# Kernel tuning notes

Hardware: AMD Instinct MI355X
Metric: run time of the kernel (lower is better)

## Reference

```python
import jax, jax.numpy as jnp
import numpy as np

D_MODEL = 2048
NUM_HEADS = 16
D_K = D_MODEL // NUM_HEADS  # 128
BATCH, SEQ = 2, 2048


def setup_inputs() -> dict:
    key = jax.random.key(0)
    ks = jax.random.split(key, 9)
    s = 0.02
    return {
        "x": jax.random.normal(ks[0], (BATCH, SEQ, D_MODEL), dtype=jnp.float32),
        "W_q": jax.random.normal(ks[1], (D_MODEL, D_MODEL), dtype=jnp.float32) * s,
        "b_q": jax.random.normal(ks[2], (D_MODEL,), dtype=jnp.float32) * s,
        "W_k": jax.random.normal(ks[3], (D_MODEL, D_K), dtype=jnp.float32) * s,
        "b_k": jax.random.normal(ks[4], (D_K,), dtype=jnp.float32) * s,
        "W_v": jax.random.normal(ks[5], (D_MODEL, D_K), dtype=jnp.float32) * s,
        "b_v": jax.random.normal(ks[6], (D_K,), dtype=jnp.float32) * s,
        "W_o": jax.random.normal(ks[7], (D_MODEL, D_MODEL), dtype=jnp.float32) * s,
        "b_o": jax.random.normal(ks[8], (D_MODEL,), dtype=jnp.float32) * s,
    }


def reference(x, W_q, b_q, W_k, b_k, W_v, b_v, W_o, b_o):
    B, S, _ = x.shape
    # Q: per-head projections -> (B, H, S, d_k)
    Q = (x @ W_q + b_q).reshape(B, S, NUM_HEADS, D_K).transpose(0, 2, 1, 3)
    # K, V: single shared head -> (B, S, d_k)
    K = x @ W_k + b_k
    V = x @ W_v + b_v
    scale = 1.0 / np.sqrt(D_K)
    # scores: (B, H, S_q, S_k); K broadcast across heads (no expand materialized)
    scores = jnp.einsum("bhqd,bkd->bhqk", Q, K) * scale
    attn = jax.nn.softmax(scores, axis=-1)
    out = jnp.einsum("bhqk,bkd->bhqd", attn, V)  # (B, H, S, d_k)
    out = out.transpose(0, 2, 1, 3).reshape(B, S, D_MODEL)
    out = out @ W_o + b_o
    K_cache = K[:, None, :, :]  # (B, 1, S, d_k)
    V_cache = V[:, None, :, :]
    return (out, K_cache, V_cache)
```

## Files before the change

kernel.cpp:

```cpp
#include <hip/hip_runtime.h>
#include <cstdint>

typedef __bf16 bf16x8 __attribute__((ext_vector_type(8)));
typedef float f32x4 __attribute__((ext_vector_type(4)));
typedef unsigned short ushort_t;

constexpr int kS  = 2048;
constexpr int kDM = 2048;
constexpr int kDK = 128;
constexpr int kNH = 16;
constexpr int kB  = 2;
constexpr int kNQKV = kDM + 2 * kDK;

__device__ __forceinline__ unsigned short f2bf(float f) {
  union { float f; unsigned u; } v; v.f = f;
  unsigned u = v.u;
  u += 0x7fffu + ((u >> 16) & 1u);
  return (unsigned short)(u >> 16);
}

__device__ __forceinline__ void gload16(const void* g, void* l) {
  __builtin_amdgcn_global_load_lds(
      (const __attribute__((address_space(1))) void*)g,
      (__attribute__((address_space(3))) void*)l, 16, 0, 0);
}

__device__ __forceinline__ void xcd_swizzle(int& bx, int& by) {
  int gx = gridDim.x;
  int nwg = gx * gridDim.y;
  int id = by * gx + bx;
  int cpx = nwg >> 3;
  int sw = (id & 7) * cpx + (id >> 3);
  bx = sw % gx;
  by = sw / gx;
}

__global__ __launch_bounds__(256) void cast_f32_bf16(const float* __restrict__ in,
                                                     ushort_t* __restrict__ out, long n) {
  long i = ((long)blockIdx.x * 256 + threadIdx.x) * 4;
  if (i >= n) return;
  float4 f = *reinterpret_cast<const float4*>(in + i);
  ushort4 o;
  o.x = f2bf(f.x); o.y = f2bf(f.y); o.z = f2bf(f.z); o.w = f2bf(f.w);
  *reinterpret_cast<ushort4*>(out + i) = o;
}

__global__ __launch_bounds__(256) void transpose_cast(const float* __restrict__ in,
                                                      ushort_t* __restrict__ out,
                                                      int R, int C) {
  __shared__ float tile[32][33];
  int c = blockIdx.x * 32 + threadIdx.x;
  int r0 = blockIdx.y * 32;
  #pragma unroll
  for (int i = threadIdx.y; i < 32; i += 8)
    tile[i][threadIdx.x] = in[(long)(r0 + i) * C + c];
  __syncthreads();
  int oc  = r0 + threadIdx.x;
  int or0 = blockIdx.x * 32;
  #pragma unroll
  for (int i = threadIdx.y; i < 32; i += 8)
    out[(long)(or0 + i) * R + oc] = f2bf(tile[threadIdx.x][i]);
}

__device__ __forceinline__ void gemm128(const ushort_t* __restrict__ A, int lda,
                                        const ushort_t* __restrict__ Bt, int ldb,
                                        int K, int row0, int col0,
                                        f32x4 (&acc)[4][4]) {
  __shared__ __align__(16) ushort_t sA[2][128 * 32];
  __shared__ __align__(16) ushort_t sB[2][128 * 32];
  int t = threadIdx.x;
  int r = t >> 2, c4 = t & 3;
  const ushort_t* gA0 = A  + (long)(row0 + r)      * lda + c4 * 8;
  const ushort_t* gA1 = A  + (long)(row0 + r + 64) * lda + c4 * 8;
  const ushort_t* gB0 = Bt + (long)(col0 + r)      * ldb + c4 * 8;
  const ushort_t* gB1 = Bt + (long)(col0 + r + 64) * ldb + c4 * 8;
  int lane = t & 63, wave = t >> 6;
  int wr = wave >> 1, wc = wave & 1;
  int lr = lane & 15, lg = lane >> 4;
  int aoff = (wr * 64 + lr) * 32 + lg * 8;
  int boff = (wc * 64 + lr) * 32 + lg * 8;

  auto stage = [&](int kk, int bb) {
    gload16(gA0 + kk, (void*)(sA[bb] + t * 8));
    gload16(gA1 + kk, (void*)(sA[bb] + 2048 + t * 8));
    gload16(gB0 + kk, (void*)(sB[bb] + t * 8));
    gload16(gB1 + kk, (void*)(sB[bb] + 2048 + t * 8));
  };
  auto comp = [&](int bb) {
    bf16x8 af[4], bg[4];
    #pragma unroll
    for (int i = 0; i < 4; i++) af[i] = *(const bf16x8*)(sA[bb] + aoff + i * 16 * 32);
    #pragma unroll
    for (int j = 0; j < 4; j++) bg[j] = *(const bf16x8*)(sB[bb] + boff + j * 16 * 32);
    #pragma unroll
    for (int i = 0; i < 4; i++)
      #pragma unroll
      for (int j = 0; j < 4; j++)
        acc[i][j] = __builtin_amdgcn_mfma_f32_16x16x32_bf16(af[i], bg[j], acc[i][j], 0, 0, 0);
  };

  stage(0, 0);
  __syncthreads();
  for (int kk = 0; kk < K; kk += 64) {
    stage(kk + 32, 1);
    comp(0);
    __syncthreads();
    if (kk + 64 < K) stage(kk + 64, 0);
    comp(1);
    __syncthreads();
  }
}

__global__ __launch_bounds__(256) void gemm_qkv(const ushort_t* __restrict__ x,
    const ushort_t* __restrict__ Wt, const float* __restrict__ bq,
    const float* __restrict__ bk, const float* __restrict__ bv,
    ushort_t* __restrict__ Qb, float* __restrict__ Kc,
    ushort_t* __restrict__ Kb, float* __restrict__ Vc, ushort_t* __restrict__ Vtb) {
  f32x4 acc[4][4] = {};
  int bx = blockIdx.x, by = blockIdx.y;
  xcd_swizzle(bx, by);
  int row0 = by * 128, col0 = bx * 128;
  gemm128(x, kDM, Wt, kDM, kDM, row0, col0, acc);
  int lane = threadIdx.x & 63, wave = threadIdx.x >> 6;
  int wr = wave >> 1, wc = wave & 1, lr = lane & 15, lg = lane >> 4;
  #pragma unroll
  for (int i = 0; i < 4; i++) {
    #pragma unroll
    for (int j = 0; j < 4; j++) {
      int col = col0 + wc * 64 + j * 16 + lr;
      float bias = (col < kDM) ? bq[col]
                 : (col < kDM + kDK) ? bk[col - kDM] : bv[col - kDM - kDK];
      #pragma unroll
      for (int rr = 0; rr < 4; rr++) {
        int row = row0 + wr * 64 + i * 16 + lg * 4 + rr;
        float v = acc[i][j][rr] + bias;
        if (col < kDM) {
          Qb[(long)row * kDM + col] = f2bf(v);
        } else if (col < kDM + kDK) {
          int c = col - kDM;
          Kc[(long)row * kDK + c] = v;
          Kb[(long)row * kDK + c] = f2bf(v);
        } else {
          int c = col - kDM - kDK;
          Vc[(long)row * kDK + c] = v;
          Vtb[((long)(row >> 11) * kDK + c) * kS + (row & 2047)] = f2bf(v);
        }
      }
    }
  }
}

__global__ __launch_bounds__(256) void gemm_out(const ushort_t* __restrict__ A,
    const ushort_t* __restrict__ Wt, const float* __restrict__ bias,
    float* __restrict__ C) {
  f32x4 acc[4][4] = {};
  int bx = blockIdx.x, by = blockIdx.y;
  xcd_swizzle(bx, by);
  int row0 = by * 128, col0 = bx * 128;
  gemm128(A, kDM, Wt, kDM, kDM, row0, col0, acc);
  int lane = threadIdx.x & 63, wave = threadIdx.x >> 6;
  int wr = wave >> 1, wc = wave & 1, lr = lane & 15, lg = lane >> 4;
  #pragma unroll
  for (int i = 0; i < 4; i++) {
    #pragma unroll
    for (int j = 0; j < 4; j++) {
      int col = col0 + wc * 64 + j * 16 + lr;
      float bv = bias[col];
      #pragma unroll
      for (int rr = 0; rr < 4; rr++) {
        int row = row0 + wr * 64 + i * 16 + lg * 4 + rr;
        C[(long)row * kDM + col] = acc[i][j][rr] + bv;
      }
    }
  }
}

__global__ __launch_bounds__(512, 2) void flash_attn(
    const ushort_t* __restrict__ Qb, const ushort_t* __restrict__ Kb,
    const ushort_t* __restrict__ Vt, ushort_t* __restrict__ Ob) {
  __shared__ __align__(16) ushort_t sK[2][64 * 128];
  __shared__ __align__(16) ushort_t sV[2][64 * 128];

  const int tid = threadIdx.x;
  const int L = tid & 63, wave = tid >> 6;
  const int lr = L & 15, lg = L >> 4;
  const int b = blockIdx.y >> 1, hg = blockIdx.y & 1;
  const int h = hg * 8 + wave;
  const int q0 = blockIdx.x * 32;

  const ushort_t* Kg = Kb + (long)b * kS * kDK;
  const ushort_t* Vg = Vt + (long)b * kDK * kS;
  const ushort_t* Qg = Qb + ((long)b * kS + q0) * kDM + h * kDK;

  bf16x8 qf[2][4];
  #pragma unroll
  for (int i = 0; i < 2; i++)
    #pragma unroll
    for (int kk = 0; kk < 4; kk++)
      qf[i][kk] = *(const bf16x8*)(Qg + (long)(i * 16 + lr) * kDM + kk * 32 + lg * 8);

  int koff[2], voff[2];
  #pragma unroll
  for (int s = 0; s < 2; s++) {
    int c = tid + s * 512;
    int f = c >> 6, cl = c & 63;
    int st = f >> 2, kk = f & 3, n = cl & 15;
    int key = (st >> 1) * 32 + (n >> 2) * 8 + (st & 1) * 4 + (n & 3);
    koff[s] = key * kDK + kk * 32 + (cl >> 4) * 8;
    int d = c >> 3, kb = (c & 7) ^ (d & 7);
    voff[s] = d * kS + kb * 8;
  }

  f32x4 accO[8][2] = {};
  float lsum[2] = {};

  constexpr float kScaleLog2e = 0.12751743f;

  auto stage = [&](int jt, int bb) {
    const ushort_t* Kt = Kg + (long)jt * 64 * kDK;
    const ushort_t* Vtg = Vg + jt * 64;
    #pragma unroll
    for (int s = 0; s < 2; s++) {
      int c8 = (tid + s * 512) * 8;
      gload16(Kt + koff[s], (void*)(sK[bb] + c8));
      gload16(Vtg + voff[s], (void*)(sV[bb] + c8));
    }
  };

  auto compute = [&](int bb) {
    #pragma unroll
    for (int u = 0; u < 2; u++) {
      f32x4 sacc[2][2] = {};
      __builtin_amdgcn_s_setprio(1);
      #pragma unroll
      for (int kk = 0; kk < 4; kk++)
        #pragma unroll
        for (int jj = 0; jj < 2; jj++) {
          bf16x8 kf = *(const bf16x8*)(sK[bb] + ((u * 2 + jj) * 4 + kk) * 512 + L * 8);
          #pragma unroll
          for (int i = 0; i < 2; i++)
            sacc[jj][i] = __builtin_amdgcn_mfma_f32_16x16x32_bf16(kf, qf[i][kk], sacc[jj][i], 0, 0, 0);
        }
      __builtin_amdgcn_s_setprio(0);

      bf16x8 pf[2];
      #pragma unroll
      for (int i = 0; i < 2; i++) {
        union { bf16x8 v; unsigned w[4]; } P;
        #pragma unroll
        for (int jj = 0; jj < 2; jj++) {
          float p0 = __builtin_amdgcn_exp2f(sacc[jj][i][0] * kScaleLog2e);
          float p1 = __builtin_amdgcn_exp2f(sacc[jj][i][1] * kScaleLog2e);
          float p2 = __builtin_amdgcn_exp2f(sacc[jj][i][2] * kScaleLog2e);
          float p3 = __builtin_amdgcn_exp2f(sacc[jj][i][3] * kScaleLog2e);
          lsum[i] += (p0 + p1) + (p2 + p3);
          asm("v_cvt_pk_bf16_f32 %0, %1, %2" : "=v"(P.w[jj * 2 + 0]) : "v"(p0), "v"(p1));
          asm("v_cvt_pk_bf16_f32 %0, %1, %2" : "=v"(P.w[jj * 2 + 1]) : "v"(p2), "v"(p3));
        }
        pf[i] = P.v;
      }

      __builtin_amdgcn_s_setprio(1);
      #pragma unroll
      for (int t = 0; t < 8; t++) {
        int kbL = (u * 4 + lg) ^ (lr & 7);
        bf16x8 vf = *(const bf16x8*)(sV[bb] + t * 1024 + lr * 64 + kbL * 8);
        #pragma unroll
        for (int i = 0; i < 2; i++)
          accO[t][i] = __builtin_amdgcn_mfma_f32_16x16x32_bf16(vf, pf[i], accO[t][i], 0, 0, 0);
      }
      __builtin_amdgcn_s_setprio(0);
    }
  };

  stage(0, 0);
  __syncthreads();
  for (int jt = 0; jt < 32; jt += 2) {
    stage(jt + 1, 1);
    compute(0);
    __syncthreads();
    if (jt + 2 < 32) stage(jt + 2, 0);
    compute(1);
    __syncthreads();
  }

  float inv[2];
  #pragma unroll
  for (int i = 0; i < 2; i++) {
    float v = lsum[i];
    v += __shfl_xor(v, 16);
    v += __shfl_xor(v, 32);
    inv[i] = 1.0f / v;
  }

  ushort_t* Og = Ob + ((long)b * kS + q0) * kDM + h * kDK;
  #pragma unroll
  for (int t = 0; t < 8; t++)
    #pragma unroll
    for (int i = 0; i < 2; i++) {
      union { ushort4 o; unsigned w[2]; } O;
      float f0 = accO[t][i][0] * inv[i];
      float f1 = accO[t][i][1] * inv[i];
      float f2 = accO[t][i][2] * inv[i];
      float f3 = accO[t][i][3] * inv[i];
      asm("v_cvt_pk_bf16_f32 %0, %1, %2" : "=v"(O.w[0]) : "v"(f0), "v"(f1));
      asm("v_cvt_pk_bf16_f32 %0, %1, %2" : "=v"(O.w[1]) : "v"(f2), "v"(f3));
      *(ushort4*)(Og + (long)(i * 16 + lr) * kDM + t * 16 + lg * 4) = O.o;
    }
}

extern "C" void kernel_launch(void* const* d_in, const int* in_sizes, int n_in,
                              void* d_out, int out_size, void* d_ws, size_t ws_size,
                              hipStream_t stream) {
  (void)in_sizes; (void)n_in; (void)out_size; (void)ws_size;
  const float* x   = (const float*)d_in[0];
  const float* W_q = (const float*)d_in[1];
  const float* b_q = (const float*)d_in[2];
  const float* W_k = (const float*)d_in[3];
  const float* b_k = (const float*)d_in[4];
  const float* W_v = (const float*)d_in[5];
  const float* b_v = (const float*)d_in[6];
  const float* W_o = (const float*)d_in[7];
  const float* b_o = (const float*)d_in[8];

  float* out = (float*)d_out;
  float* Kc  = out + (long)kB * kS * kDM;
  float* Vc  = Kc  + (long)kB * kS * kDK;

  char* w = (char*)d_ws;
  ushort_t* x_bf   = (ushort_t*)w;  w += 16777216;
  ushort_t* Wall_t = (ushort_t*)w;  w += (size_t)kNQKV*kDM*2;
  ushort_t* Wo_t   = (ushort_t*)w;  w += 8388608;
  ushort_t* Q_bf   = (ushort_t*)w;  w += 16777216;
  ushort_t* K_bf   = (ushort_t*)w;  w += 1048576;
  ushort_t* Vt_bf  = (ushort_t*)w;  w += 1048576;
  ushort_t* O_bf   = (ushort_t*)w;  w += 16777216;

  dim3 blk(256);
  dim3 tblk(32, 8);

  cast_f32_bf16<<<dim3(8192), blk, 0, stream>>>(x, x_bf, (long)kB * kS * kDM);
  transpose_cast<<<dim3(64, 64), tblk, 0, stream>>>(W_q, Wall_t, kDM, kDM);
  transpose_cast<<<dim3(4, 64),  tblk, 0, stream>>>(W_k, Wall_t + (long)kDM * kDM, kDM, kDK);
  transpose_cast<<<dim3(4, 64),  tblk, 0, stream>>>(W_v, Wall_t + (long)(kDM + kDK) * kDM, kDM, kDK);
  transpose_cast<<<dim3(64, 64), tblk, 0, stream>>>(W_o, Wo_t, kDM, kDM);

  gemm_qkv<<<dim3(kNQKV / 128, kB * kS / 128), blk, 0, stream>>>(
      x_bf, Wall_t, b_q, b_k, b_v, Q_bf, Kc, K_bf, Vc, Vt_bf);

  flash_attn<<<dim3(kS / 32, kB * 2), dim3(512), 0, stream>>>(Q_bf, K_bf, Vt_bf, O_bf);

  gemm_out<<<dim3(kDM / 128, kB * kS / 128), blk, 0, stream>>>(O_bf, Wo_t, b_o, out);
}
```

Baseline: 311.5 us.

## Merge prep kernels, deepen GEMM K-tile to 64, widen attention KV tile to 128

Five cast/transpose launches are fused into a single prep kernel to cut launch overhead. The shared GEMM helper now stages 64-wide K slices in an MFMA-fragment-ordered LDS layout, which halves the number of barriers and lets each fragment load be a contiguous per-lane read. Flash attention stages 128 keys per tile with a 16-way XOR swizzle on V, halving barriers per key sweep. That doubles the attention LDS to 128KB and drops occupancy to one block per CU.

```diff
diff --git a/kernel.cpp b/kernel.cpp
--- a/kernel.cpp
+++ b/kernel.cpp
@@ -35,77 +35,98 @@
   by = sw / gx;
 }
 
-__global__ __launch_bounds__(256) void cast_f32_bf16(const float* __restrict__ in,
-                                                     ushort_t* __restrict__ out, long n) {
-  long i = ((long)blockIdx.x * 256 + threadIdx.x) * 4;
-  if (i >= n) return;
-  float4 f = *reinterpret_cast<const float4*>(in + i);
-  ushort4 o;
-  o.x = f2bf(f.x); o.y = f2bf(f.y); o.z = f2bf(f.z); o.w = f2bf(f.w);
-  *reinterpret_cast<ushort4*>(out + i) = o;
-}
-
-__global__ __launch_bounds__(256) void transpose_cast(const float* __restrict__ in,
-                                                      ushort_t* __restrict__ out,
-                                                      int R, int C) {
+__global__ __launch_bounds__(256) void prep(
+    const float* __restrict__ x, ushort_t* __restrict__ x_bf,
+    const float* __restrict__ Wq, const float* __restrict__ Wk,
+    const float* __restrict__ Wv, const float* __restrict__ Wo,
+    ushort_t* __restrict__ Wall_t, ushort_t* __restrict__ Wo_t) {
   __shared__ float tile[32][33];
-  int c = blockIdx.x * 32 + threadIdx.x;
-  int r0 = blockIdx.y * 32;
-  #pragma unroll
-  for (int i = threadIdx.y; i < 32; i += 8)
-    tile[i][threadIdx.x] = in[(long)(r0 + i) * C + c];
+  int bid = blockIdx.x, tid = threadIdx.x;
+  if (bid < 8192) {
+    long i = ((long)bid * 256 + tid) * 4;
+    float4 f = *reinterpret_cast<const float4*>(x + i);
+    ushort4 o;
+    o.x = f2bf(f.x); o.y = f2bf(f.y); o.z = f2bf(f.z); o.w = f2bf(f.w);
+    *reinterpret_cast<ushort4*>(x_bf + i) = o;
+    return;
+  }
+  int id = bid - 8192;
+  const float* in; ushort_t* out; int C, bx, by;
+  const int R = 2048;
+  if (id < 4096)      { in = Wq; out = Wall_t;                      C = 2048; bx = id & 63; by = id >> 6; }
+  else if (id < 4352) { id -= 4096; in = Wk; out = Wall_t + (long)kDM * kDM;            C = 128; bx = id & 3; by = id >> 2; }
+  else if (id < 4608) { id -= 4352; in = Wv; out = Wall_t + (long)(kDM + kDK) * kDM;    C = 128; bx = id & 3; by = id >> 2; }
+  else                { id -= 4608; in = Wo; out = Wo_t;            C = 2048; bx = id & 63; by = id >> 6; }
+  int tx = tid & 31, ty = tid >> 5;
+  int c = bx * 32 + tx;
+  int r0 = by * 32;
+  #pragma unroll
+  for (int i = ty; i < 32; i += 8)
+    tile[i][tx] = in[(long)(r0 + i) * C + c];
   __syncthreads();
-  int oc  = r0 + threadIdx.x;
-  int or0 = blockIdx.x * 32;
-  #pragma unroll
-  for (int i = threadIdx.y; i < 32; i += 8)
-    out[(long)(or0 + i) * R + oc] = f2bf(tile[threadIdx.x][i]);
+  int oc  = r0 + tx;
+  int or0 = bx * 32;
+  #pragma unroll
+  for (int i = ty; i < 32; i += 8)
+    out[(long)(or0 + i) * R + oc] = f2bf(tile[tx][i]);
 }
 
 __device__ __forceinline__ void gemm128(const ushort_t* __restrict__ A, int lda,
                                         const ushort_t* __restrict__ Bt, int ldb,
                                         int K, int row0, int col0,
                                         f32x4 (&acc)[4][4]) {
-  __shared__ __align__(16) ushort_t sA[2][128 * 32];
-  __shared__ __align__(16) ushort_t sB[2][128 * 32];
+  __shared__ __align__(16) ushort_t sA[2][128 * 64];
+  __shared__ __align__(16) ushort_t sB[2][128 * 64];
   int t = threadIdx.x;
-  int r = t >> 2, c4 = t & 3;
-  const ushort_t* gA0 = A  + (long)(row0 + r)      * lda + c4 * 8;
-  const ushort_t* gA1 = A  + (long)(row0 + r + 64) * lda + c4 * 8;
-  const ushort_t* gB0 = Bt + (long)(col0 + r)      * ldb + c4 * 8;
-  const ushort_t* gB1 = Bt + (long)(col0 + r + 64) * ldb + c4 * 8;
   int lane = t & 63, wave = t >> 6;
   int wr = wave >> 1, wc = wave & 1;
   int lr = lane & 15, lg = lane >> 4;
-  int aoff = (wr * 64 + lr) * 32 + lg * 8;
-  int boff = (wc * 64 + lr) * 32 + lg * 8;
-
-  auto stage = [&](int kk, int bb) {
-    gload16(gA0 + kk, (void*)(sA[bb] + t * 8));
-    gload16(gA1 + kk, (void*)(sA[bb] + 2048 + t * 8));
-    gload16(gB0 + kk, (void*)(sB[bb] + t * 8));
-    gload16(gB1 + kk, (void*)(sB[bb] + 2048 + t * 8));
+
+  long ga[4], gb[4];
+  #pragma unroll
+  for (int s = 0; s < 4; s++) {
+    int c = t + s * 256;
+    int f = c >> 6, cl = c & 63;
+    int it = f >> 1, k2 = f & 1;
+    int row = it * 16 + (cl & 15);
+    int col = k2 * 32 + (cl >> 4) * 8;
+    ga[s] = (long)(row0 + row) * lda + col;
+    gb[s] = (long)(col0 + row) * ldb + col;
+  }
+
+  auto stage = [&](int k0, int bb) {
+    #pragma unroll
+    for (int s = 0; s < 4; s++) {
+      int c8 = (t + s * 256) * 8;
+      gload16(A  + ga[s] + k0, (void*)(sA[bb] + c8));
+      gload16(Bt + gb[s] + k0, (void*)(sB[bb] + c8));
+    }
   };
   auto comp = [&](int bb) {
-    bf16x8 af[4], bg[4];
-    #pragma unroll
-    for (int i = 0; i < 4; i++) af[i] = *(const bf16x8*)(sA[bb] + aoff + i * 16 * 32);
-    #pragma unroll
-    for (int j = 0; j < 4; j++) bg[j] = *(const bf16x8*)(sB[bb] + boff + j * 16 * 32);
-    #pragma unroll
-    for (int i = 0; i < 4; i++)
+    #pragma unroll
+    for (int k2 = 0; k2 < 2; k2++) {
+      bf16x8 af[4], bg[4];
+      #pragma unroll
+      for (int i = 0; i < 4; i++)
+        af[i] = *(const bf16x8*)(sA[bb] + (((wr * 4 + i) * 2 + k2) * 64 + lane) * 8);
       #pragma unroll
       for (int j = 0; j < 4; j++)
-        acc[i][j] = __builtin_amdgcn_mfma_f32_16x16x32_bf16(af[i], bg[j], acc[i][j], 0, 0, 0);
+        bg[j] = *(const bf16x8*)(sB[bb] + (((wc * 4 + j) * 2 + k2) * 64 + lane) * 8);
+      #pragma unroll
+      for (int i = 0; i < 4; i++)
+        #pragma unroll
+        for (int j = 0; j < 4; j++)
+          acc[i][j] = __builtin_amdgcn_mfma_f32_16x16x32_bf16(af[i], bg[j], acc[i][j], 0, 0, 0);
+    }
   };
 
   stage(0, 0);
   __syncthreads();
-  for (int kk = 0; kk < K; kk += 64) {
-    stage(kk + 32, 1);
+  for (int k0 = 0; k0 < K; k0 += 128) {
+    stage(k0 + 64, 1);
     comp(0);
     __syncthreads();
-    if (kk + 64 < K) stage(kk + 64, 0);
+    if (k0 + 128 < K) stage(k0 + 128, 0);
     comp(1);
     __syncthreads();
   }
@@ -175,11 +196,11 @@
   }
 }
 
-__global__ __launch_bounds__(512, 2) void flash_attn(
+__global__ __launch_bounds__(512, 1) void flash_attn(
     const ushort_t* __restrict__ Qb, const ushort_t* __restrict__ Kb,
     const ushort_t* __restrict__ Vt, ushort_t* __restrict__ Ob) {
-  __shared__ __align__(16) ushort_t sK[2][64 * 128];
-  __shared__ __align__(16) ushort_t sV[2][64 * 128];
+  __shared__ __align__(16) ushort_t sK[2][128 * 128];
+  __shared__ __align__(16) ushort_t sV[2][128 * 128];
 
   const int tid = threadIdx.x;
   const int L = tid & 63, wave = tid >> 6;
@@ -199,15 +220,15 @@
     for (int kk = 0; kk < 4; kk++)
       qf[i][kk] = *(const bf16x8*)(Qg + (long)(i * 16 + lr) * kDM + kk * 32 + lg * 8);
 
-  int koff[2], voff[2];
-  #pragma unroll
-  for (int s = 0; s < 2; s++) {
+  int koff[4], voff[4];
+  #pragma unroll
+  for (int s = 0; s < 4; s++) {
     int c = tid + s * 512;
     int f = c >> 6, cl = c & 63;
     int st = f >> 2, kk = f & 3, n = cl & 15;
     int key = (st >> 1) * 32 + (n >> 2) * 8 + (st & 1) * 4 + (n & 3);
     koff[s] = key * kDK + kk * 32 + (cl >> 4) * 8;
-    int d = c >> 3, kb = (c & 7) ^ (d & 7);
+    int d = c >> 4, kb = (c & 15) ^ (d & 15);
     voff[s] = d * kS + kb * 8;
   }
 
@@ -217,10 +238,10 @@
   constexpr float kScaleLog2e = 0.12751743f;
 
   auto stage = [&](int jt, int bb) {
-    const ushort_t* Kt = Kg + (long)jt * 64 * kDK;
-    const ushort_t* Vtg = Vg + jt * 64;
-    #pragma unroll
-    for (int s = 0; s < 2; s++) {
+    const ushort_t* Kt = Kg + (long)jt * 128 * kDK;
+    const ushort_t* Vtg = Vg + jt * 128;
+    #pragma unroll
+    for (int s = 0; s < 4; s++) {
       int c8 = (tid + s * 512) * 8;
       gload16(Kt + koff[s], (void*)(sK[bb] + c8));
       gload16(Vtg + voff[s], (void*)(sV[bb] + c8));
@@ -229,7 +250,7 @@
 
   auto compute = [&](int bb) {
     #pragma unroll
-    for (int u = 0; u < 2; u++) {
+    for (int u = 0; u < 4; u++) {
       f32x4 sacc[2][2] = {};
       __builtin_amdgcn_s_setprio(1);
       #pragma unroll
@@ -263,8 +284,8 @@
       __builtin_amdgcn_s_setprio(1);
       #pragma unroll
       for (int t = 0; t < 8; t++) {
-        int kbL = (u * 4 + lg) ^ (lr & 7);
-        bf16x8 vf = *(const bf16x8*)(sV[bb] + t * 1024 + lr * 64 + kbL * 8);
+        int kbL = (u * 4 + lg) ^ lr;
+        bf16x8 vf = *(const bf16x8*)(sV[bb] + t * 2048 + lr * 128 + kbL * 8);
         #pragma unroll
         for (int i = 0; i < 2; i++)
           accO[t][i] = __builtin_amdgcn_mfma_f32_16x16x32_bf16(vf, pf[i], accO[t][i], 0, 0, 0);
@@ -275,11 +296,11 @@
 
   stage(0, 0);
   __syncthreads();
-  for (int jt = 0; jt < 32; jt += 2) {
+  for (int jt = 0; jt < 16; jt += 2) {
     stage(jt + 1, 1);
     compute(0);
     __syncthreads();
-    if (jt + 2 < 32) stage(jt + 2, 0);
+    if (jt + 2 < 16) stage(jt + 2, 0);
     compute(1);
     __syncthreads();
   }
@@ -337,13 +358,8 @@
   ushort_t* O_bf   = (ushort_t*)w;  w += 16777216;
 
   dim3 blk(256);
-  dim3 tblk(32, 8);
-
-  cast_f32_bf16<<<dim3(8192), blk, 0, stream>>>(x, x_bf, (long)kB * kS * kDM);
-  transpose_cast<<<dim3(64, 64), tblk, 0, stream>>>(W_q, Wall_t, kDM, kDM);
-  transpose_cast<<<dim3(4, 64),  tblk, 0, stream>>>(W_k, Wall_t + (long)kDM * kDM, kDM, kDK);
-  transpose_cast<<<dim3(4, 64),  tblk, 0, stream>>>(W_v, Wall_t + (long)(kDM + kDK) * kDM, kDM, kDK);
-  transpose_cast<<<dim3(64, 64), tblk, 0, stream>>>(W_o, Wo_t, kDM, kDM);
+
+  prep<<<dim3(16896), blk, 0, stream>>>(x, x_bf, W_q, W_k, W_v, W_o, Wall_t, Wo_t);
 
   gemm_qkv<<<dim3(kNQKV / 128, kB * kS / 128), blk, 0, stream>>>(
       x_bf, Wall_t, b_q, b_k, b_v, Q_bf, Kc, K_bf, Vc, Vt_bf);
```

Measured after the change: 395.3 us. 1.27x slower.
